# Kernel optimization log

Hardware: AMD Instinct MI355X
Metric: run time of the kernel (lower is better)

## Reference

```python
import jax, jax.numpy as jnp
import numpy as np

N = 100000      # num_nodes
E = 1_600_000   # edges (avg degree 16)
D_IN = 128
D_H = 128
D_OUT = 128


def setup_inputs() -> dict:
    key = jax.random.key(0)
    ks = jax.random.split(key, 11)
    x = jax.random.normal(ks[0], (N, D_IN), dtype=jnp.float32)
    edge_index = jax.random.randint(ks[1], (2, E), 0, N, dtype=jnp.int32)
    s_in = 1.0 / np.sqrt(D_IN)
    s_h = 1.0 / np.sqrt(D_H)
    return {
        "x": x,
        "edge_index": edge_index,
        "W_neigh1": jax.random.uniform(ks[2], (D_H, D_IN), jnp.float32, -s_in, s_in),
        "b_neigh1": jax.random.uniform(ks[3], (D_H,), jnp.float32, -s_in, s_in),
        "W_self1": jax.random.uniform(ks[4], (D_H, D_IN), jnp.float32, -s_in, s_in),
        "b_self1": jax.random.uniform(ks[5], (D_H,), jnp.float32, -s_in, s_in),
        "W_neigh2": jax.random.uniform(ks[6], (D_OUT, D_H), jnp.float32, -s_h, s_h),
        "b_neigh2": jax.random.uniform(ks[7], (D_OUT,), jnp.float32, -s_h, s_h),
        "W_self2": jax.random.uniform(ks[8], (D_OUT, D_H), jnp.float32, -s_h, s_h),
        "b_self2": jax.random.uniform(ks[9], (D_OUT,), jnp.float32, -s_h, s_h),
    }


def reference(x, edge_index, W_neigh1, b_neigh1, W_self1, b_self1,
              W_neigh2, b_neigh2, W_self2, b_self2):
    src, dst = edge_index[0], edge_index[1]
    n = x.shape[0]
    # row-normalized adjacency: deg over dst (row index), clamped to >= 1
    deg = jax.ops.segment_sum(jnp.ones(src.shape[0], x.dtype), dst, num_segments=n)
    inv_deg = 1.0 / jnp.maximum(deg, 1.0)  # [N]

    def agg(h):  # mean aggregation: (A_rownorm @ h)
        return jax.ops.segment_sum(h[src], dst, num_segments=n) * inv_deg[:, None]

    h1 = agg(x) @ W_neigh1.T + b_neigh1 + x @ W_self1.T + b_self1
    h1 = jax.nn.relu(h1)
    # dropout omitted (eval-mode / deterministic reference)
    h2 = agg(h1) @ W_neigh2.T + b_neigh2 + h1 @ W_self2.T + b_self2
    return h2
```

## Files before the change

kernel.cpp:

```cpp
#include <hip/hip_runtime.h>
#include <hip/hip_bf16.h>


typedef __attribute__((ext_vector_type(8))) short short8;
typedef __attribute__((ext_vector_type(4))) float float4_;

#define NBMAX 512

__device__ __forceinline__ unsigned short f2bf(float f) {
    unsigned int u = __float_as_uint(f);
    unsigned int r = (u + 0x7FFFu + ((u >> 16) & 1u)) >> 16;
    return (unsigned short)r;
}

__global__ __launch_bounds__(256) void bucket_count(const int* __restrict__ dst, int E, int NB,
                                                    int* __restrict__ hist) {
    __shared__ int h[NBMAX];
    int tid = threadIdx.x;
    for (int b = tid; b < NB; b += 256) h[b] = 0;
    __syncthreads();
    int base = blockIdx.x * 4096;
    for (int i = 0; i < 16; i++) {
        int e = base + i * 256 + tid;
        if (e < E) atomicAdd(&h[dst[e] >> 8], 1);
    }
    __syncthreads();
    int* out = hist + (size_t)blockIdx.x * NB;
    for (int b = tid; b < NB; b += 256) out[b] = h[b];
}

__global__ __launch_bounds__(256) void blk_scan(const int* __restrict__ hist, int nblk, int NB,
                                                int* __restrict__ baseT,
                                                int* __restrict__ bucketCnt) {
    __shared__ int sd[256];
    __shared__ int carryS;
    int b = blockIdx.x, tid = threadIdx.x;
    if (tid == 0) carryS = 0;
    __syncthreads();
    for (int c0 = 0; c0 < nblk; c0 += 256) {
        int i = c0 + tid;
        int v = (i < nblk) ? hist[(size_t)i * NB + b] : 0;
        sd[tid] = v;
        __syncthreads();
        for (int off = 1; off < 256; off <<= 1) {
            int x = sd[tid];
            int y = (tid >= off) ? sd[tid - off] : 0;
            __syncthreads();
            sd[tid] = x + y;
            __syncthreads();
        }
        int carry = carryS;
        if (i < nblk) baseT[(size_t)i * NB + b] = carry + sd[tid] - v;
        __syncthreads();
        if (tid == 255) carryS = carry + sd[255];
        __syncthreads();
    }
    if (tid == 0) bucketCnt[b] = carryS;
}

__global__ __launch_bounds__(512) void bucket_scan(const int* __restrict__ bucketCnt, int NB,
                                                   int* __restrict__ bucketOffs) {
    __shared__ int sd[512];
    int t = threadIdx.x;
    int v = (t < NB) ? bucketCnt[t] : 0;
    sd[t] = v;
    __syncthreads();
    for (int off = 1; off < 512; off <<= 1) {
        int x = sd[t];
        int y = (t >= off) ? sd[t - off] : 0;
        __syncthreads();
        sd[t] = x + y;
        __syncthreads();
    }
    int excl = sd[t] - v;
    if (t <= NB) bucketOffs[t] = excl;
}

__global__ __launch_bounds__(256) void partition_wprep(
    const int* __restrict__ src, const int* __restrict__ dst, int E, int NB, int partBlocks,
    const int* __restrict__ bucketOffs, const int* __restrict__ baseT,
    unsigned int* __restrict__ bucketBuf,
    const float* __restrict__ Wn1, const float* __restrict__ Ws1,
    const float* __restrict__ bn1, const float* __restrict__ bs1,
    const float* __restrict__ Wn2, const float* __restrict__ Ws2,
    const float* __restrict__ bn2, const float* __restrict__ bs2,
    unsigned short* __restrict__ Bpre, float* __restrict__ biasPre) {
    int tid = threadIdx.x;
    if ((int)blockIdx.x >= partBlocks) {
        int wb = blockIdx.x - partBlocks;
        int l = wb >> 4;
        const float* Wn = l ? Wn2 : Wn1;
        const float* Ws = l ? Ws2 : Ws1;
        int fi = (wb & 15) * 256 + tid;
        int kt = fi >> 9;
        int nt = (fi >> 6) & 7;
        int lane = fi & 63;
        int o = nt * 16 + (lane & 15);
        int k = kt * 32 + (lane >> 4) * 8;
        const float* srcp = (k < 128) ? (Wn + o * 128 + k) : (Ws + o * 128 + (k - 128));
        short8 v;
#pragma unroll
        for (int j = 0; j < 8; j++) v[j] = (short)f2bf(srcp[j]);
        ((short8*)(Bpre + (size_t)l * 32768))[fi] = v;
        if ((wb & 15) == 0 && tid < 128) {
            const float* bn = l ? bn2 : bn1;
            const float* bs = l ? bs2 : bs1;
            biasPre[l * 128 + tid] = bn[tid] + bs[tid];
        }
        return;
    }
    __shared__ int cnt[NBMAX];
    __shared__ int gb[NBMAX];
    for (int b = tid; b < NB; b += 256) {
        cnt[b] = 0;
        gb[b] = bucketOffs[b] + baseT[(size_t)blockIdx.x * NB + b];
    }
    __syncthreads();
    int eb = blockIdx.x * 4096;
    unsigned int pk[16];
    int bk[16], rk[16];
    for (int i = 0; i < 16; i++) {
        int e = eb + i * 256 + tid;
        if (e < E) {
            int d = dst[e];
            bk[i] = d >> 8;
            pk[i] = (unsigned)src[e] | ((unsigned)(d & 255) << 24);
            rk[i] = atomicAdd(&cnt[bk[i]], 1);
        } else {
            bk[i] = -1;
        }
    }
    __syncthreads();
    for (int i = 0; i < 16; i++)
        if (bk[i] >= 0) bucketBuf[gb[bk[i]] + rk[i]] = pk[i];
}

__global__ __launch_bounds__(256) void csrbuild_cvt(
    const unsigned int* __restrict__ bucketBuf, const int* __restrict__ bucketOffs,
    int N, int NB, int* __restrict__ deg, int* __restrict__ offs, int* __restrict__ sortedSrc,
    const float* __restrict__ xin, unsigned int* __restrict__ xb, int n2) {
    int tid = threadIdx.x;
    if ((int)blockIdx.x >= NB) {
        int cb = blockIdx.x - NB;
        int base = cb * 2048 + tid;
        if (xb) {
#pragma unroll
            for (int i = 0; i < 8; i++) {
                int t = base + i * 256;
                if (t < n2) {
                    float2 v = ((const float2*)xin)[t];
                    xb[t] = (unsigned)f2bf(v.x) | ((unsigned)f2bf(v.y) << 16);
                }
            }
        }
        return;
    }
    __shared__ int h[256];
    __shared__ int sc[256];
    __shared__ int cur[256];
    int b = blockIdx.x;
    int n0 = b << 8;
    int bo = bucketOffs[b];
    int cnt = bucketOffs[b + 1] - bo;
    h[tid] = 0;
    __syncthreads();
    for (int i = tid; i < cnt; i += 256) atomicAdd(&h[bucketBuf[bo + i] >> 24], 1);
    __syncthreads();
    int v = h[tid];
    sc[tid] = v;
    __syncthreads();
    for (int off = 1; off < 256; off <<= 1) {
        int x = sc[tid];
        int y = (tid >= off) ? sc[tid - off] : 0;
        __syncthreads();
        sc[tid] = x + y;
        __syncthreads();
    }
    int excl = sc[tid] - v;
    cur[tid] = bo + excl;
    int n = n0 + tid;
    if (n < N) {
        deg[n] = v;
        offs[n] = bo + excl;
    }
    __syncthreads();
    for (int i = tid; i < cnt; i += 256) {
        unsigned int pv = bucketBuf[bo + i];
        int pos = atomicAdd(&cur[pv >> 24], 1);
        sortedSrc[pos] = (int)(pv & 0xFFFFFFu);
    }
}

__global__ __launch_bounds__(256) void agg_bf16_kernel(
    const unsigned int* __restrict__ srcFeats,
    const int* __restrict__ deg, const int* __restrict__ offs,
    const int* __restrict__ sortedSrc,
    unsigned int* __restrict__ dst, int Nn) {
    int wave = threadIdx.x >> 6, lane = threadIdx.x & 63;
    int n = blockIdx.x * 4 + wave;
    if (n >= Nn) return;
    int d = deg[n], st = offs[n];
    float a0 = 0.f, a1 = 0.f;
    int j = 0;
    for (; j + 16 <= d; j += 16) {
        unsigned int uu[16];
#pragma unroll
        for (int u = 0; u < 16; u++) {
            int s = __builtin_amdgcn_readfirstlane(sortedSrc[st + j + u]);
            uu[u] = (srcFeats + (size_t)s * 64)[lane];
        }
#pragma unroll
        for (int u = 0; u < 16; u++) {
            a0 += __uint_as_float(uu[u] << 16);
            a1 += __uint_as_float(uu[u] & 0xFFFF0000u);
        }
    }
    for (; j + 8 <= d; j += 8) {
        unsigned int uu[8];
#pragma unroll
        for (int u = 0; u < 8; u++) {
            int s = __builtin_amdgcn_readfirstlane(sortedSrc[st + j + u]);
            uu[u] = (srcFeats + (size_t)s * 64)[lane];
        }
#pragma unroll
        for (int u = 0; u < 8; u++) {
            a0 += __uint_as_float(uu[u] << 16);
            a1 += __uint_as_float(uu[u] & 0xFFFF0000u);
        }
    }
    for (; j < d; j++) {
        int s = __builtin_amdgcn_readfirstlane(sortedSrc[st + j]);
        unsigned int u = (srcFeats + (size_t)s * 64)[lane];
        a0 += __uint_as_float(u << 16);
        a1 += __uint_as_float(u & 0xFFFF0000u);
    }
    float inv = 1.0f / (float)max(d, 1);
    dst[(size_t)n * 64 + lane] = (unsigned)f2bf(a0 * inv) | ((unsigned)f2bf(a1 * inv) << 16);
}

__global__ __launch_bounds__(256) void agg_f32_kernel(
    const float* __restrict__ srcFeats,
    const int* __restrict__ deg, const int* __restrict__ offs,
    const int* __restrict__ sortedSrc,
    unsigned int* __restrict__ dst, int Nn) {
    int wave = threadIdx.x >> 6, lane = threadIdx.x & 63;
    int n = blockIdx.x * 4 + wave;
    if (n >= Nn) return;
    int d = deg[n], st = offs[n];
    float a0 = 0.f, a1 = 0.f;
    int j = 0;
    for (; j + 8 <= d; j += 8) {
        float2 v[8];
#pragma unroll
        for (int u = 0; u < 8; u++) {
            int s = __builtin_amdgcn_readfirstlane(sortedSrc[st + j + u]);
            v[u] = ((const float2*)(srcFeats + (size_t)s * 128))[lane];
        }
#pragma unroll
        for (int u = 0; u < 8; u++) {
            a0 += v[u].x;
            a1 += v[u].y;
        }
    }
    for (; j < d; j++) {
        int s = __builtin_amdgcn_readfirstlane(sortedSrc[st + j]);
        float2 v = ((const float2*)(srcFeats + (size_t)s * 128))[lane];
        a0 += v.x;
        a1 += v.y;
    }
    float inv = 1.0f / (float)max(d, 1);
    dst[(size_t)n * 64 + lane] = (unsigned)f2bf(a0 * inv) | ((unsigned)f2bf(a1 * inv) << 16);
}

__global__ __launch_bounds__(256) void gemm_kernel(
    const unsigned short* __restrict__ Aagg, const void* Aself,
    const unsigned short* __restrict__ Bpre, const float* __restrict__ biasPre,
    void* Out, int relu, int selfF32, int outBf16, int Nrows) {
    __shared__ unsigned short ldsB[8 * 8 * 64 * 8];
    __shared__ float biasS[128];
    int tid = threadIdx.x;

#pragma unroll
    for (int i = 0; i < 16; i++) {
        int fi = tid + 256 * i;
        ((short8*)ldsB)[fi] = ((const short8*)Bpre)[fi];
    }
    if (tid < 128) biasS[tid] = biasPre[tid];
    __syncthreads();

    int wave = tid >> 6, lane = tid & 63;
    int quad = lane >> 4, mr = lane & 15;
    int rowBase = blockIdx.x * 128 + wave * 32;

    float4_ acc[2][8];
    float4_ z = {0.f, 0.f, 0.f, 0.f};
    for (int mt = 0; mt < 2; mt++)
        for (int nt = 0; nt < 8; nt++) acc[mt][nt] = z;

    for (int kt = 0; kt < 8; kt++) {
        int kk = (kt & 3) * 32 + quad * 8;
        short8 a[2];
        for (int mt = 0; mt < 2; mt++) {
            int row = rowBase + mt * 16 + mr;
            if (row >= Nrows) row = Nrows - 1;
            if (kt < 4) {
                a[mt] = *(const short8*)(Aagg + (size_t)row * 128 + kk);
            } else if (selfF32) {
                const float* p = (const float*)Aself + (size_t)row * 128 + kk;
                float4_ f0 = *(const float4_*)p;
                float4_ f1 = *(const float4_*)(p + 4);
                short8 t;
#pragma unroll
                for (int j = 0; j < 4; j++) {
                    t[j] = (short)f2bf(f0[j]);
                    t[4 + j] = (short)f2bf(f1[j]);
                }
                a[mt] = t;
            } else {
                a[mt] = *(const short8*)((const unsigned short*)Aself + (size_t)row * 128 + kk);
            }
        }
        for (int nt = 0; nt < 8; nt++) {
            short8 b = *(const short8*)(ldsB + ((size_t)(kt * 8 + nt) * 64 + lane) * 8);
            acc[0][nt] = __builtin_amdgcn_mfma_f32_16x16x32_bf16(a[0], b, acc[0][nt], 0, 0, 0);
            acc[1][nt] = __builtin_amdgcn_mfma_f32_16x16x32_bf16(a[1], b, acc[1][nt], 0, 0, 0);
        }
    }

    for (int mt = 0; mt < 2; mt++) {
        for (int nt = 0; nt < 8; nt++) {
            int col = nt * 16 + mr;
            float bv = biasS[col];
            for (int r = 0; r < 4; r++) {
                int row = rowBase + mt * 16 + quad * 4 + r;
                if (row < Nrows) {
                    float v = acc[mt][nt][r] + bv;
                    if (relu) v = fmaxf(v, 0.f);
                    if (outBf16)
                        ((unsigned short*)Out)[(size_t)row * 128 + col] = f2bf(v);
                    else
                        ((float*)Out)[(size_t)row * 128 + col] = v;
                }
            }
        }
    }
}

extern "C" void kernel_launch(void* const* d_in, const int* in_sizes, int n_in,
                              void* d_out, int out_size, void* d_ws, size_t ws_size,
                              hipStream_t stream) {
    const float* x = (const float*)d_in[0];
    const int* ei = (const int*)d_in[1];
    const float* Wn1 = (const float*)d_in[2];
    const float* bn1 = (const float*)d_in[3];
    const float* Ws1 = (const float*)d_in[4];
    const float* bs1 = (const float*)d_in[5];
    const float* Wn2 = (const float*)d_in[6];
    const float* bn2 = (const float*)d_in[7];
    const float* Ws2 = (const float*)d_in[8];
    const float* bs2 = (const float*)d_in[9];

    const int N = in_sizes[0] / 128;
    const int E = in_sizes[1] / 2;
    const int* srcI = ei;
    const int* dstI = ei + E;
    const int NB = (N + 255) >> 8;
    const int ebBlocks = (E + 4095) / 4096;

    char* ws = (char*)d_ws;
    size_t off = 0;
    auto alloc = [&](size_t bytes) -> void* {
        void* p = ws + off;
        off += (bytes + 255) & ~(size_t)255;
        return p;
    };
    int* deg = (int*)alloc((size_t)N * 4);
    int* offs = (int*)alloc((size_t)N * 4);
    int* bucketCnt = (int*)alloc((NBMAX + 1) * 4);
    int* bucketOffs = (int*)alloc((NBMAX + 1) * 4);
    int* hist = (int*)alloc((size_t)ebBlocks * NB * 4);
    int* baseT = (int*)alloc((size_t)ebBlocks * NB * 4);
    unsigned short* Bpre = (unsigned short*)alloc(2 * 32768 * 2);
    float* biasPre = (float*)alloc(2 * 128 * 4);
    int* sortedSrc = (int*)alloc((size_t)E * 4);
    unsigned short* Aagg = (unsigned short*)alloc((size_t)N * 128 * 2);
    size_t baseNeed = off;
    size_t bf16Buf = ((size_t)N * 128 * 2 + 255) & ~(size_t)255;
    bool bigWs = (ws_size >= baseNeed + 2 * bf16Buf);
    unsigned int* xb = nullptr;
    unsigned short* h1b = nullptr;
    if (bigWs) {
        xb = (unsigned int*)alloc((size_t)N * 128 * 2);
        h1b = (unsigned short*)alloc((size_t)N * 128 * 2);
    }
    unsigned int* bucketBuf = (unsigned int*)Aagg;

    int n2 = N * 64;
    int cvtBlocks = bigWs ? (n2 + 2047) / 2048 : 0;
    bucket_count<<<ebBlocks, 256, 0, stream>>>(dstI, E, NB, hist);
    blk_scan<<<NB, 256, 0, stream>>>(hist, ebBlocks, NB, baseT, bucketCnt);
    bucket_scan<<<1, 512, 0, stream>>>(bucketCnt, NB, bucketOffs);
    partition_wprep<<<ebBlocks + 32, 256, 0, stream>>>(
        srcI, dstI, E, NB, ebBlocks, bucketOffs, baseT, bucketBuf,
        Wn1, Ws1, bn1, bs1, Wn2, Ws2, bn2, bs2, Bpre, biasPre);
    csrbuild_cvt<<<NB + cvtBlocks, 256, 0, stream>>>(bucketBuf, bucketOffs, N, NB, deg, offs,
                                                     sortedSrc, x, xb, n2);

    int aggBlocks = (N + 3) / 4;
    int gemmBlocks = (N + 127) / 128;

    if (bigWs) {
        agg_bf16_kernel<<<aggBlocks, 256, 0, stream>>>(xb, deg, offs, sortedSrc,
                                                       (unsigned int*)Aagg, N);
        gemm_kernel<<<gemmBlocks, 256, 0, stream>>>(Aagg, xb, Bpre, biasPre, h1b, 1, 0, 1, N);
        agg_bf16_kernel<<<aggBlocks, 256, 0, stream>>>((const unsigned int*)h1b, deg, offs,
                                                       sortedSrc, (unsigned int*)Aagg, N);
        gemm_kernel<<<gemmBlocks, 256, 0, stream>>>(Aagg, h1b, Bpre + 32768, biasPre + 128,
                                                    d_out, 0, 0, 0, N);
    } else {
        float* h1 = (float*)d_out;
        agg_f32_kernel<<<aggBlocks, 256, 0, stream>>>(x, deg, offs, sortedSrc,
                                                      (unsigned int*)Aagg, N);
        gemm_kernel<<<gemmBlocks, 256, 0, stream>>>(Aagg, x, Bpre, biasPre, h1, 1, 1, 0, N);
        agg_f32_kernel<<<aggBlocks, 256, 0, stream>>>(h1, deg, offs, sortedSrc,
                                                      (unsigned int*)Aagg, N);
        gemm_kernel<<<gemmBlocks, 256, 0, stream>>>(Aagg, h1, Bpre + 32768, biasPre + 128,
                                                    d_out, 0, 1, 0, N);
    }
}
```

Before: 347.1 us.

## Fuse CSR build kernels into one persistent kernel with grid barriers

Merges the five preprocessing launches (bucket count, block scan, bucket scan, partition with weight prep, CSR build with x conversion) into a single persistent kernel of G blocks that uses atomic-counter grid barriers between phases. This removes per-launch overhead and the idle tails between small kernels. The grid barrier assumes every block is co-resident, which is not guaranteed by the launch. Phases that ran wide before now loop over chunks with fewer blocks, which may reduce parallelism.

```diff
diff --git a/kernel.cpp b/kernel.cpp
--- a/kernel.cpp
+++ b/kernel.cpp
@@ -13,81 +13,51 @@
     return (unsigned short)r;
 }
 
-__global__ __launch_bounds__(256) void bucket_count(const int* __restrict__ dst, int E, int NB,
-                                                    int* __restrict__ hist) {
-    __shared__ int h[NBMAX];
-    int tid = threadIdx.x;
-    for (int b = tid; b < NB; b += 256) h[b] = 0;
+__device__ __forceinline__ void gbar(int* bar, int id, int G) {
     __syncthreads();
-    int base = blockIdx.x * 4096;
-    for (int i = 0; i < 16; i++) {
-        int e = base + i * 256 + tid;
-        if (e < E) atomicAdd(&h[dst[e] >> 8], 1);
+    if (threadIdx.x == 0) {
+        __threadfence();
+        atomicAdd(&bar[id], 1);
+        while (atomicAdd(&bar[id], 0) < G) __builtin_amdgcn_s_sleep(16);
+        __threadfence();
     }
     __syncthreads();
-    int* out = hist + (size_t)blockIdx.x * NB;
-    for (int b = tid; b < NB; b += 256) out[b] = h[b];
-}
-
-__global__ __launch_bounds__(256) void blk_scan(const int* __restrict__ hist, int nblk, int NB,
-                                                int* __restrict__ baseT,
-                                                int* __restrict__ bucketCnt) {
-    __shared__ int sd[256];
-    __shared__ int carryS;
-    int b = blockIdx.x, tid = threadIdx.x;
-    if (tid == 0) carryS = 0;
-    __syncthreads();
-    for (int c0 = 0; c0 < nblk; c0 += 256) {
-        int i = c0 + tid;
-        int v = (i < nblk) ? hist[(size_t)i * NB + b] : 0;
-        sd[tid] = v;
-        __syncthreads();
-        for (int off = 1; off < 256; off <<= 1) {
-            int x = sd[tid];
-            int y = (tid >= off) ? sd[tid - off] : 0;
-            __syncthreads();
-            sd[tid] = x + y;
-            __syncthreads();
-        }
-        int carry = carryS;
-        if (i < nblk) baseT[(size_t)i * NB + b] = carry + sd[tid] - v;
-        __syncthreads();
-        if (tid == 255) carryS = carry + sd[255];
-        __syncthreads();
-    }
-    if (tid == 0) bucketCnt[b] = carryS;
-}
-
-__global__ __launch_bounds__(512) void bucket_scan(const int* __restrict__ bucketCnt, int NB,
-                                                   int* __restrict__ bucketOffs) {
-    __shared__ int sd[512];
-    int t = threadIdx.x;
-    int v = (t < NB) ? bucketCnt[t] : 0;
-    sd[t] = v;
-    __syncthreads();
-    for (int off = 1; off < 512; off <<= 1) {
-        int x = sd[t];
-        int y = (t >= off) ? sd[t - off] : 0;
-        __syncthreads();
-        sd[t] = x + y;
-        __syncthreads();
-    }
-    int excl = sd[t] - v;
-    if (t <= NB) bucketOffs[t] = excl;
-}
-
-__global__ __launch_bounds__(256) void partition_wprep(
-    const int* __restrict__ src, const int* __restrict__ dst, int E, int NB, int partBlocks,
-    const int* __restrict__ bucketOffs, const int* __restrict__ baseT,
+}
+
+__global__ __launch_bounds__(256, 4) void mega_csr(
+    const int* __restrict__ src, const int* __restrict__ dst, int E, int N, int NB, int CHK,
+    int G, int* __restrict__ bar, int* __restrict__ hist, int* __restrict__ baseT,
+    int* __restrict__ bucketCnt, int* __restrict__ bucketOffs,
     unsigned int* __restrict__ bucketBuf,
+    int* __restrict__ deg, int* __restrict__ offs, int* __restrict__ sortedSrc,
+    const float* __restrict__ xin, unsigned int* __restrict__ xb, int n2,
     const float* __restrict__ Wn1, const float* __restrict__ Ws1,
     const float* __restrict__ bn1, const float* __restrict__ bs1,
     const float* __restrict__ Wn2, const float* __restrict__ Ws2,
     const float* __restrict__ bn2, const float* __restrict__ bs2,
     unsigned short* __restrict__ Bpre, float* __restrict__ biasPre) {
+    __shared__ int h[NBMAX];
+    __shared__ int sc[256];
+    __shared__ int cur[256];
+    __shared__ int gb[NBMAX];
     int tid = threadIdx.x;
-    if ((int)blockIdx.x >= partBlocks) {
-        int wb = blockIdx.x - partBlocks;
+    int bb = blockIdx.x;
+
+    for (int c = bb; c < CHK; c += G) {
+        for (int b = tid; b < NB; b += 256) h[b] = 0;
+        __syncthreads();
+        int base = c * 4096;
+        for (int i = 0; i < 16; i++) {
+            int e = base + i * 256 + tid;
+            if (e < E) atomicAdd(&h[dst[e] >> 8], 1);
+        }
+        __syncthreads();
+        int* out = hist + (size_t)c * NB;
+        for (int b = tid; b < NB; b += 256) out[b] = h[b];
+        __syncthreads();
+    }
+    if (bb < 32) {
+        int wb = bb;
         int l = wb >> 4;
         const float* Wn = l ? Wn2 : Wn1;
         const float* Ws = l ? Ws2 : Ws1;
@@ -107,87 +77,130 @@
             const float* bs = l ? bs2 : bs1;
             biasPre[l * 128 + tid] = bn[tid] + bs[tid];
         }
-        return;
-    }
-    __shared__ int cnt[NBMAX];
-    __shared__ int gb[NBMAX];
-    for (int b = tid; b < NB; b += 256) {
-        cnt[b] = 0;
-        gb[b] = bucketOffs[b] + baseT[(size_t)blockIdx.x * NB + b];
-    }
-    __syncthreads();
-    int eb = blockIdx.x * 4096;
-    unsigned int pk[16];
-    int bk[16], rk[16];
-    for (int i = 0; i < 16; i++) {
-        int e = eb + i * 256 + tid;
-        if (e < E) {
-            int d = dst[e];
-            bk[i] = d >> 8;
-            pk[i] = (unsigned)src[e] | ((unsigned)(d & 255) << 24);
-            rk[i] = atomicAdd(&cnt[bk[i]], 1);
-        } else {
-            bk[i] = -1;
-        }
-    }
-    __syncthreads();
-    for (int i = 0; i < 16; i++)
-        if (bk[i] >= 0) bucketBuf[gb[bk[i]] + rk[i]] = pk[i];
-}
-
-__global__ __launch_bounds__(256) void csrbuild_cvt(
-    const unsigned int* __restrict__ bucketBuf, const int* __restrict__ bucketOffs,
-    int N, int NB, int* __restrict__ deg, int* __restrict__ offs, int* __restrict__ sortedSrc,
-    const float* __restrict__ xin, unsigned int* __restrict__ xb, int n2) {
-    int tid = threadIdx.x;
-    if ((int)blockIdx.x >= NB) {
-        int cb = blockIdx.x - NB;
-        int base = cb * 2048 + tid;
-        if (xb) {
-#pragma unroll
-            for (int i = 0; i < 8; i++) {
-                int t = base + i * 256;
-                if (t < n2) {
-                    float2 v = ((const float2*)xin)[t];
-                    xb[t] = (unsigned)f2bf(v.x) | ((unsigned)f2bf(v.y) << 16);
-                }
+    }
+    if (xb) {
+        for (int t = bb * 256 + tid; t < n2; t += G * 256) {
+            float2 v = ((const float2*)xin)[t];
+            xb[t] = (unsigned)f2bf(v.x) | ((unsigned)f2bf(v.y) << 16);
+        }
+    }
+    gbar(bar, 0, G);
+
+    if (bb < NB) {
+        int carry = 0;
+        for (int c0 = 0; c0 < CHK; c0 += 256) {
+            int i = c0 + tid;
+            int v = (i < CHK) ? hist[(size_t)i * NB + bb] : 0;
+            sc[tid] = v;
+            __syncthreads();
+            for (int off = 1; off < 256; off <<= 1) {
+                int x = sc[tid];
+                int y = (tid >= off) ? sc[tid - off] : 0;
+                __syncthreads();
+                sc[tid] = x + y;
+                __syncthreads();
             }
-        }
-        return;
-    }
-    __shared__ int h[256];
-    __shared__ int sc[256];
-    __shared__ int cur[256];
-    int b = blockIdx.x;
-    int n0 = b << 8;
-    int bo = bucketOffs[b];
-    int cnt = bucketOffs[b + 1] - bo;
-    h[tid] = 0;
-    __syncthreads();
-    for (int i = tid; i < cnt; i += 256) atomicAdd(&h[bucketBuf[bo + i] >> 24], 1);
-    __syncthreads();
-    int v = h[tid];
-    sc[tid] = v;
-    __syncthreads();
-    for (int off = 1; off < 256; off <<= 1) {
-        int x = sc[tid];
-        int y = (tid >= off) ? sc[tid - off] : 0;
-        __syncthreads();
-        sc[tid] = x + y;
-        __syncthreads();
-    }
-    int excl = sc[tid] - v;
-    cur[tid] = bo + excl;
-    int n = n0 + tid;
-    if (n < N) {
-        deg[n] = v;
-        offs[n] = bo + excl;
-    }
-    __syncthreads();
-    for (int i = tid; i < cnt; i += 256) {
-        unsigned int pv = bucketBuf[bo + i];
-        int pos = atomicAdd(&cur[pv >> 24], 1);
-        sortedSrc[pos] = (int)(pv & 0xFFFFFFu);
+            if (i < CHK) baseT[(size_t)i * NB + bb] = carry + sc[tid] - v;
+            carry += sc[255];
+            __syncthreads();
+        }
+        if (tid == 0) bucketCnt[bb] = carry;
+    }
+    gbar(bar, 1, G);
+
+    if (bb == 0) {
+        int v0 = (tid < NB) ? bucketCnt[tid] : 0;
+        int j = 256 + tid;
+        int v1 = (j < NB) ? bucketCnt[j] : 0;
+        sc[tid] = v0;
+        __syncthreads();
+        for (int off = 1; off < 256; off <<= 1) {
+            int x = sc[tid];
+            int y = (tid >= off) ? sc[tid - off] : 0;
+            __syncthreads();
+            sc[tid] = x + y;
+            __syncthreads();
+        }
+        int inc0 = sc[tid];
+        int tot0 = sc[255];
+        __syncthreads();
+        sc[tid] = v1;
+        __syncthreads();
+        for (int off = 1; off < 256; off <<= 1) {
+            int x = sc[tid];
+            int y = (tid >= off) ? sc[tid - off] : 0;
+            __syncthreads();
+            sc[tid] = x + y;
+            __syncthreads();
+        }
+        int inc1 = sc[tid];
+        int tot1 = sc[255];
+        __syncthreads();
+        if (tid < NB) bucketOffs[tid] = inc0 - v0;
+        if (j < NB) bucketOffs[j] = tot0 + inc1 - v1;
+        if (tid == 0) bucketOffs[NB] = tot0 + tot1;
+    }
+    gbar(bar, 2, G);
+
+    for (int c = bb; c < CHK; c += G) {
+        for (int b = tid; b < NB; b += 256) {
+            h[b] = 0;
+            gb[b] = bucketOffs[b] + baseT[(size_t)c * NB + b];
+        }
+        __syncthreads();
+        int eb = c * 4096;
+        unsigned int pk[16];
+        int bk[16], rk[16];
+        for (int i = 0; i < 16; i++) {
+            int e = eb + i * 256 + tid;
+            if (e < E) {
+                int d = dst[e];
+                bk[i] = d >> 8;
+                pk[i] = (unsigned)src[e] | ((unsigned)(d & 255) << 24);
+                rk[i] = atomicAdd(&h[bk[i]], 1);
+            } else {
+                bk[i] = -1;
+            }
+        }
+        __syncthreads();
+        for (int i = 0; i < 16; i++)
+            if (bk[i] >= 0) bucketBuf[gb[bk[i]] + rk[i]] = pk[i];
+        __syncthreads();
+    }
+    gbar(bar, 3, G);
+
+    if (bb < NB) {
+        int b = bb;
+        int n0 = b << 8;
+        int bo = bucketOffs[b];
+        int cnt = bucketOffs[b + 1] - bo;
+        h[tid] = 0;
+        __syncthreads();
+        for (int i = tid; i < cnt; i += 256) atomicAdd(&h[bucketBuf[bo + i] >> 24], 1);
+        __syncthreads();
+        int v = h[tid];
+        sc[tid] = v;
+        __syncthreads();
+        for (int off = 1; off < 256; off <<= 1) {
+            int x = sc[tid];
+            int y = (tid >= off) ? sc[tid - off] : 0;
+            __syncthreads();
+            sc[tid] = x + y;
+            __syncthreads();
+        }
+        int excl = sc[tid] - v;
+        cur[tid] = bo + excl;
+        int n = n0 + tid;
+        if (n < N) {
+            deg[n] = v;
+            offs[n] = bo + excl;
+        }
+        __syncthreads();
+        for (int i = tid; i < cnt; i += 256) {
+            unsigned int pv = bucketBuf[bo + i];
+            int pos = atomicAdd(&cur[pv >> 24], 1);
+            sortedSrc[pos] = (int)(pv & 0xFFFFFFu);
+        }
     }
 }
 
@@ -365,7 +378,11 @@
     const int* srcI = ei;
     const int* dstI = ei + E;
     const int NB = (N + 255) >> 8;
-    const int ebBlocks = (E + 4095) / 4096;
+    const int CHK = (E + 4095) / 4096;
+
+    int G = NB > 32 ? NB : 32;
+    if (CHK > G) G = CHK;
+    if (G > 1024) G = 1024;
 
     char* ws = (char*)d_ws;
     size_t off = 0;
@@ -378,8 +395,9 @@
     int* offs = (int*)alloc((size_t)N * 4);
     int* bucketCnt = (int*)alloc((NBMAX + 1) * 4);
     int* bucketOffs = (int*)alloc((NBMAX + 1) * 4);
-    int* hist = (int*)alloc((size_t)ebBlocks * NB * 4);
-    int* baseT = (int*)alloc((size_t)ebBlocks * NB * 4);
+    int* bar = (int*)alloc(16 * 4);
+    int* hist = (int*)alloc((size_t)CHK * NB * 4);
+    int* baseT = (int*)alloc((size_t)CHK * NB * 4);
     unsigned short* Bpre = (unsigned short*)alloc(2 * 32768 * 2);
     float* biasPre = (float*)alloc(2 * 128 * 4);
     int* sortedSrc = (int*)alloc((size_t)E * 4);
@@ -396,15 +414,11 @@
     unsigned int* bucketBuf = (unsigned int*)Aagg;
 
     int n2 = N * 64;
-    int cvtBlocks = bigWs ? (n2 + 2047) / 2048 : 0;
-    bucket_count<<<ebBlocks, 256, 0, stream>>>(dstI, E, NB, hist);
-    blk_scan<<<NB, 256, 0, stream>>>(hist, ebBlocks, NB, baseT, bucketCnt);
-    bucket_scan<<<1, 512, 0, stream>>>(bucketCnt, NB, bucketOffs);
-    partition_wprep<<<ebBlocks + 32, 256, 0, stream>>>(
-        srcI, dstI, E, NB, ebBlocks, bucketOffs, baseT, bucketBuf,
-        Wn1, Ws1, bn1, bs1, Wn2, Ws2, bn2, bs2, Bpre, biasPre);
-    csrbuild_cvt<<<NB + cvtBlocks, 256, 0, stream>>>(bucketBuf, bucketOffs, N, NB, deg, offs,
-                                                     sortedSrc, x, xb, n2);
+    hipMemsetAsync(bar, 0, 64, stream);
+    mega_csr<<<G, 256, 0, stream>>>(srcI, dstI, E, N, NB, CHK, G, bar, hist, baseT,
+                                    bucketCnt, bucketOffs, bucketBuf, deg, offs, sortedSrc,
+                                    x, xb, n2, Wn1, Ws1, bn1, bs1, Wn2, Ws2, bn2, bs2,
+                                    Bpre, biasPre);
 
     int aggBlocks = (N + 3) / 4;
     int gemmBlocks = (N + 127) / 128;
```

Result: slower. 519.5 us (+49.7%).

## Fuse aggregation and GEMM into persistent kernels with grid barrier; inline bucket scan

Applied to the files above, without the earlier changes.

Replaces each separate aggregation and GEMM launch pair with one persistent kernel of 512 blocks. Each block first gathers mean-aggregated neighbour features, then meets the others at a global atomic barrier, then runs the MFMA GEMM tiles. The single-block bucket_scan launch is removed: every partition and CSR-build block now recomputes the bucket prefix sum itself in shared memory. This cuts launch count and inter-kernel gaps. In exchange it adds redundant scan work, a spin barrier that needs all 512 blocks resident at once (deadlock risk otherwise), and persistent-grid load imbalance.

```diff
diff --git a/kernel.cpp b/kernel.cpp
--- a/kernel.cpp
+++ b/kernel.cpp
@@ -11,6 +11,17 @@
     unsigned int u = __float_as_uint(f);
     unsigned int r = (u + 0x7FFFu + ((u >> 16) & 1u)) >> 16;
     return (unsigned short)r;
+}
+
+__device__ __forceinline__ void gbar(int* bar, int id, int G) {
+    __syncthreads();
+    if (threadIdx.x == 0) {
+        __threadfence();
+        atomicAdd(&bar[id], 1);
+        while (atomicAdd(&bar[id], 0) < G) __builtin_amdgcn_s_sleep(16);
+        __threadfence();
+    }
+    __syncthreads();
 }
 
 __global__ __launch_bounds__(256) void bucket_count(const int* __restrict__ dst, int E, int NB,
@@ -31,10 +42,12 @@
 
 __global__ __launch_bounds__(256) void blk_scan(const int* __restrict__ hist, int nblk, int NB,
                                                 int* __restrict__ baseT,
-                                                int* __restrict__ bucketCnt) {
+                                                int* __restrict__ bucketCnt,
+                                                int* __restrict__ bar) {
     __shared__ int sd[256];
     __shared__ int carryS;
     int b = blockIdx.x, tid = threadIdx.x;
+    if (b == 0 && tid < 16) bar[tid] = 0;
     if (tid == 0) carryS = 0;
     __syncthreads();
     for (int c0 = 0; c0 < nblk; c0 += 256) {
@@ -58,27 +71,31 @@
     if (tid == 0) bucketCnt[b] = carryS;
 }
 
-__global__ __launch_bounds__(512) void bucket_scan(const int* __restrict__ bucketCnt, int NB,
-                                                   int* __restrict__ bucketOffs) {
-    __shared__ int sd[512];
-    int t = threadIdx.x;
-    int v = (t < NB) ? bucketCnt[t] : 0;
-    sd[t] = v;
-    __syncthreads();
-    for (int off = 1; off < 512; off <<= 1) {
-        int x = sd[t];
-        int y = (t >= off) ? sd[t - off] : 0;
-        __syncthreads();
-        sd[t] = x + y;
-        __syncthreads();
-    }
-    int excl = sd[t] - v;
-    if (t <= NB) bucketOffs[t] = excl;
+__device__ __forceinline__ void scan_buckets(const int* __restrict__ bucketCnt, int NB,
+                                             int* bOffs, int* sc) {
+    int tid = threadIdx.x;
+    int b0 = 2 * tid, b1 = 2 * tid + 1;
+    int c0 = (b0 < NB) ? bucketCnt[b0] : 0;
+    int c1 = (b1 < NB) ? bucketCnt[b1] : 0;
+    int ts = c0 + c1;
+    sc[tid] = ts;
+    __syncthreads();
+    for (int off = 1; off < 256; off <<= 1) {
+        int x = sc[tid];
+        int y = (tid >= off) ? sc[tid - off] : 0;
+        __syncthreads();
+        sc[tid] = x + y;
+        __syncthreads();
+    }
+    int excl = sc[tid] - ts;
+    bOffs[b0] = excl;
+    bOffs[b1] = excl + c0;
+    __syncthreads();
 }
 
 __global__ __launch_bounds__(256) void partition_wprep(
     const int* __restrict__ src, const int* __restrict__ dst, int E, int NB, int partBlocks,
-    const int* __restrict__ bucketOffs, const int* __restrict__ baseT,
+    const int* __restrict__ bucketCnt, const int* __restrict__ baseT,
     unsigned int* __restrict__ bucketBuf,
     const float* __restrict__ Wn1, const float* __restrict__ Ws1,
     const float* __restrict__ bn1, const float* __restrict__ bs1,
@@ -110,10 +127,13 @@
         return;
     }
     __shared__ int cnt[NBMAX];
+    __shared__ int bOffs[NBMAX];
     __shared__ int gb[NBMAX];
+    __shared__ int sc[256];
+    scan_buckets(bucketCnt, NB, bOffs, sc);
     for (int b = tid; b < NB; b += 256) {
         cnt[b] = 0;
-        gb[b] = bucketOffs[b] + baseT[(size_t)blockIdx.x * NB + b];
+        gb[b] = bOffs[b] + baseT[(size_t)blockIdx.x * NB + b];
     }
     __syncthreads();
     int eb = blockIdx.x * 4096;
@@ -136,7 +156,7 @@
 }
 
 __global__ __launch_bounds__(256) void csrbuild_cvt(
-    const unsigned int* __restrict__ bucketBuf, const int* __restrict__ bucketOffs,
+    const unsigned int* __restrict__ bucketBuf, const int* __restrict__ bucketCnt,
     int N, int NB, int* __restrict__ deg, int* __restrict__ offs, int* __restrict__ sortedSrc,
     const float* __restrict__ xin, unsigned int* __restrict__ xb, int n2) {
     int tid = threadIdx.x;
@@ -155,13 +175,15 @@
         }
         return;
     }
+    __shared__ int bOffs[NBMAX];
     __shared__ int h[256];
     __shared__ int sc[256];
     __shared__ int cur[256];
+    scan_buckets(bucketCnt, NB, bOffs, sc);
     int b = blockIdx.x;
     int n0 = b << 8;
-    int bo = bucketOffs[b];
-    int cnt = bucketOffs[b + 1] - bo;
+    int bo = bOffs[b];
+    int cnt = bucketCnt[b];
     h[tid] = 0;
     __syncthreads();
     for (int i = tid; i < cnt; i += 256) atomicAdd(&h[bucketBuf[bo + i] >> 24], 1);
@@ -191,51 +213,110 @@
     }
 }
 
-__global__ __launch_bounds__(256) void agg_bf16_kernel(
-    const unsigned int* __restrict__ srcFeats,
+__global__ __launch_bounds__(256) void fused_agg_gemm(
+    const unsigned int* __restrict__ table,
     const int* __restrict__ deg, const int* __restrict__ offs,
-    const int* __restrict__ sortedSrc,
-    unsigned int* __restrict__ dst, int Nn) {
-    int wave = threadIdx.x >> 6, lane = threadIdx.x & 63;
-    int n = blockIdx.x * 4 + wave;
-    if (n >= Nn) return;
-    int d = deg[n], st = offs[n];
-    float a0 = 0.f, a1 = 0.f;
-    int j = 0;
-    for (; j + 16 <= d; j += 16) {
-        unsigned int uu[16];
-#pragma unroll
-        for (int u = 0; u < 16; u++) {
-            int s = __builtin_amdgcn_readfirstlane(sortedSrc[st + j + u]);
-            uu[u] = (srcFeats + (size_t)s * 64)[lane];
-        }
-#pragma unroll
-        for (int u = 0; u < 16; u++) {
-            a0 += __uint_as_float(uu[u] << 16);
-            a1 += __uint_as_float(uu[u] & 0xFFFF0000u);
-        }
-    }
-    for (; j + 8 <= d; j += 8) {
-        unsigned int uu[8];
-#pragma unroll
-        for (int u = 0; u < 8; u++) {
-            int s = __builtin_amdgcn_readfirstlane(sortedSrc[st + j + u]);
-            uu[u] = (srcFeats + (size_t)s * 64)[lane];
-        }
-#pragma unroll
-        for (int u = 0; u < 8; u++) {
-            a0 += __uint_as_float(uu[u] << 16);
-            a1 += __uint_as_float(uu[u] & 0xFFFF0000u);
-        }
-    }
-    for (; j < d; j++) {
-        int s = __builtin_amdgcn_readfirstlane(sortedSrc[st + j]);
-        unsigned int u = (srcFeats + (size_t)s * 64)[lane];
-        a0 += __uint_as_float(u << 16);
-        a1 += __uint_as_float(u & 0xFFFF0000u);
-    }
-    float inv = 1.0f / (float)max(d, 1);
-    dst[(size_t)n * 64 + lane] = (unsigned)f2bf(a0 * inv) | ((unsigned)f2bf(a1 * inv) << 16);
+    const int* __restrict__ sortedSrc, unsigned int* __restrict__ Aagg,
+    const unsigned short* __restrict__ Bpre, const float* __restrict__ biasPre,
+    void* Out, int relu, int outBf16, int Nn, int G, int* __restrict__ bar, int barId) {
+    __shared__ unsigned short ldsB[32768];
+    __shared__ float biasS[128];
+    int tid = threadIdx.x;
+
+#pragma unroll
+    for (int i = 0; i < 16; i++) {
+        int fi = tid + 256 * i;
+        ((short8*)ldsB)[fi] = ((const short8*)Bpre)[fi];
+    }
+    if (tid < 128) biasS[tid] = biasPre[tid];
+
+    int wave = tid >> 6, lane = tid & 63;
+
+    for (int n = blockIdx.x * 4 + wave; n < Nn; n += G * 4) {
+        int d = deg[n], st = offs[n];
+        float a0 = 0.f, a1 = 0.f;
+        int j = 0;
+        for (; j + 16 <= d; j += 16) {
+            unsigned int uu[16];
+#pragma unroll
+            for (int u = 0; u < 16; u++) {
+                int s = __builtin_amdgcn_readfirstlane(sortedSrc[st + j + u]);
+                uu[u] = (table + (size_t)s * 64)[lane];
+            }
+#pragma unroll
+            for (int u = 0; u < 16; u++) {
+                a0 += __uint_as_float(uu[u] << 16);
+                a1 += __uint_as_float(uu[u] & 0xFFFF0000u);
+            }
+        }
+        for (; j + 8 <= d; j += 8) {
+            unsigned int uu[8];
+#pragma unroll
+            for (int u = 0; u < 8; u++) {
+                int s = __builtin_amdgcn_readfirstlane(sortedSrc[st + j + u]);
+                uu[u] = (table + (size_t)s * 64)[lane];
+            }
+#pragma unroll
+            for (int u = 0; u < 8; u++) {
+                a0 += __uint_as_float(uu[u] << 16);
+                a1 += __uint_as_float(uu[u] & 0xFFFF0000u);
+            }
+        }
+        for (; j < d; j++) {
+            int s = __builtin_amdgcn_readfirstlane(sortedSrc[st + j]);
+            unsigned int u = (table + (size_t)s * 64)[lane];
+            a0 += __uint_as_float(u << 16);
+            a1 += __uint_as_float(u & 0xFFFF0000u);
+        }
+        float inv = 1.0f / (float)max(d, 1);
+        Aagg[(size_t)n * 64 + lane] = (unsigned)f2bf(a0 * inv) | ((unsigned)f2bf(a1 * inv) << 16);
+    }
+
+    gbar(bar, barId, G);
+
+    int quad = lane >> 4, mr = lane & 15;
+    const unsigned short* Aa = (const unsigned short*)Aagg;
+    const unsigned short* As = (const unsigned short*)table;
+    int nTiles = (Nn + 127) >> 7;
+    for (int t = blockIdx.x; t < nTiles; t += G) {
+        int rowBase = t * 128 + wave * 32;
+        float4_ acc[2][8];
+        float4_ z = {0.f, 0.f, 0.f, 0.f};
+        for (int mt = 0; mt < 2; mt++)
+            for (int nt = 0; nt < 8; nt++) acc[mt][nt] = z;
+        for (int kt = 0; kt < 8; kt++) {
+            int kk = (kt & 3) * 32 + quad * 8;
+            short8 a[2];
+            for (int mt = 0; mt < 2; mt++) {
+                int row = rowBase + mt * 16 + mr;
+                if (row >= Nn) row = Nn - 1;
+                const unsigned short* ap = (kt < 4) ? Aa : As;
+                a[mt] = *(const short8*)(ap + (size_t)row * 128 + kk);
+            }
+            for (int nt = 0; nt < 8; nt++) {
+                short8 b = *(const short8*)(ldsB + ((size_t)(kt * 8 + nt) * 64 + lane) * 8);
+                acc[0][nt] = __builtin_amdgcn_mfma_f32_16x16x32_bf16(a[0], b, acc[0][nt], 0, 0, 0);
+                acc[1][nt] = __builtin_amdgcn_mfma_f32_16x16x32_bf16(a[1], b, acc[1][nt], 0, 0, 0);
+            }
+        }
+        for (int mt = 0; mt < 2; mt++) {
+            for (int nt = 0; nt < 8; nt++) {
+                int col = nt * 16 + mr;
+                float bv = biasS[col];
+                for (int r = 0; r < 4; r++) {
+                    int row = rowBase + mt * 16 + quad * 4 + r;
+                    if (row < Nn) {
+                        float v = acc[mt][nt][r] + bv;
+                        if (relu) v = fmaxf(v, 0.f);
+                        if (outBf16)
+                            ((unsigned short*)Out)[(size_t)row * 128 + col] = f2bf(v);
+                        else
+                            ((float*)Out)[(size_t)row * 128 + col] = v;
+                    }
+                }
+            }
+        }
+    }
 }
 
 __global__ __launch_bounds__(256) void agg_f32_kernel(
@@ -279,7 +360,6 @@
     __shared__ unsigned short ldsB[8 * 8 * 64 * 8];
     __shared__ float biasS[128];
     int tid = threadIdx.x;
-
 #pragma unroll
     for (int i = 0; i < 16; i++) {
         int fi = tid + 256 * i;
@@ -326,7 +406,6 @@
             acc[1][nt] = __builtin_amdgcn_mfma_f32_16x16x32_bf16(a[1], b, acc[1][nt], 0, 0, 0);
         }
     }
-
     for (int mt = 0; mt < 2; mt++) {
         for (int nt = 0; nt < 8; nt++) {
             int col = nt * 16 + mr;
@@ -377,7 +456,7 @@
     int* deg = (int*)alloc((size_t)N * 4);
     int* offs = (int*)alloc((size_t)N * 4);
     int* bucketCnt = (int*)alloc((NBMAX + 1) * 4);
-    int* bucketOffs = (int*)alloc((NBMAX + 1) * 4);
+    int* bar = (int*)alloc(16 * 4);
     int* hist = (int*)alloc((size_t)ebBlocks * NB * 4);
     int* baseT = (int*)alloc((size_t)ebBlocks * NB * 4);
     unsigned short* Bpre = (unsigned short*)alloc(2 * 32768 * 2);
@@ -398,26 +477,24 @@
     int n2 = N * 64;
     int cvtBlocks = bigWs ? (n2 + 2047) / 2048 : 0;
     bucket_count<<<ebBlocks, 256, 0, stream>>>(dstI, E, NB, hist);
-    blk_scan<<<NB, 256, 0, stream>>>(hist, ebBlocks, NB, baseT, bucketCnt);
-    bucket_scan<<<1, 512, 0, stream>>>(bucketCnt, NB, bucketOffs);
+    blk_scan<<<NB, 256, 0, stream>>>(hist, ebBlocks, NB, baseT, bucketCnt, bar);
     partition_wprep<<<ebBlocks + 32, 256, 0, stream>>>(
-        srcI, dstI, E, NB, ebBlocks, bucketOffs, baseT, bucketBuf,
+        srcI, dstI, E, NB, ebBlocks, bucketCnt, baseT, bucketBuf,
         Wn1, Ws1, bn1, bs1, Wn2, Ws2, bn2, bs2, Bpre, biasPre);
-    csrbuild_cvt<<<NB + cvtBlocks, 256, 0, stream>>>(bucketBuf, bucketOffs, N, NB, deg, offs,
+    csrbuild_cvt<<<NB + cvtBlocks, 256, 0, stream>>>(bucketBuf, bucketCnt, N, NB, deg, offs,
                                                      sortedSrc, x, xb, n2);
 
-    int aggBlocks = (N + 3) / 4;
-    int gemmBlocks = (N + 127) / 128;
-
     if (bigWs) {
-        agg_bf16_kernel<<<aggBlocks, 256, 0, stream>>>(xb, deg, offs, sortedSrc,
-                                                       (unsigned int*)Aagg, N);
-        gemm_kernel<<<gemmBlocks, 256, 0, stream>>>(Aagg, xb, Bpre, biasPre, h1b, 1, 0, 1, N);
-        agg_bf16_kernel<<<aggBlocks, 256, 0, stream>>>((const unsigned int*)h1b, deg, offs,
-                                                       sortedSrc, (unsigned int*)Aagg, N);
-        gemm_kernel<<<gemmBlocks, 256, 0, stream>>>(Aagg, h1b, Bpre + 32768, biasPre + 128,
-                                                    d_out, 0, 0, 0, N);
+        const int G = 512;
+        fused_agg_gemm<<<G, 256, 0, stream>>>(xb, deg, offs, sortedSrc,
+                                              (unsigned int*)Aagg, Bpre, biasPre,
+                                              h1b, 1, 1, N, G, bar, 0);
+        fused_agg_gemm<<<G, 256, 0, stream>>>((const unsigned int*)h1b, deg, offs, sortedSrc,
+                                              (unsigned int*)Aagg, Bpre + 32768, biasPre + 128,
+                                              d_out, 0, 0, N, G, bar, 1);
     } else {
+        int aggBlocks = (N + 3) / 4;
+        int gemmBlocks = (N + 127) / 128;
         float* h1 = (float*)d_out;
         agg_f32_kernel<<<aggBlocks, 256, 0, stream>>>(x, deg, offs, sortedSrc,
                                                       (unsigned int*)Aagg, N);
```

After: 613.5 us. 76.8% more time.

## Fold bucket scan into partition/CSR kernels and preload GEMM A fragments

Applied to the files above, without the earlier changes.

Drops the single-block bucket_scan launch. Each partition and CSR-build block now recomputes the bucket prefix sum redundantly in shared memory from bucketCnt. This removes one kernel launch and its serialization point, at the cost of extra per-block scan work. Separately, the GEMM kernel now loads all A fragments for the eight k-steps up front and fully unrolls the MFMA loop, so loads can issue early, at the cost of more registers.

```diff
diff --git a/kernel.cpp b/kernel.cpp
--- a/kernel.cpp
+++ b/kernel.cpp
@@ -58,27 +58,31 @@
     if (tid == 0) bucketCnt[b] = carryS;
 }
 
-__global__ __launch_bounds__(512) void bucket_scan(const int* __restrict__ bucketCnt, int NB,
-                                                   int* __restrict__ bucketOffs) {
-    __shared__ int sd[512];
-    int t = threadIdx.x;
-    int v = (t < NB) ? bucketCnt[t] : 0;
-    sd[t] = v;
-    __syncthreads();
-    for (int off = 1; off < 512; off <<= 1) {
-        int x = sd[t];
-        int y = (t >= off) ? sd[t - off] : 0;
-        __syncthreads();
-        sd[t] = x + y;
-        __syncthreads();
-    }
-    int excl = sd[t] - v;
-    if (t <= NB) bucketOffs[t] = excl;
+__device__ __forceinline__ void scan_buckets(const int* __restrict__ bucketCnt, int NB,
+                                             int* bOffs, int* sc) {
+    int tid = threadIdx.x;
+    int b0 = 2 * tid, b1 = 2 * tid + 1;
+    int c0 = (b0 < NB) ? bucketCnt[b0] : 0;
+    int c1 = (b1 < NB) ? bucketCnt[b1] : 0;
+    int ts = c0 + c1;
+    sc[tid] = ts;
+    __syncthreads();
+    for (int off = 1; off < 256; off <<= 1) {
+        int x = sc[tid];
+        int y = (tid >= off) ? sc[tid - off] : 0;
+        __syncthreads();
+        sc[tid] = x + y;
+        __syncthreads();
+    }
+    int excl = sc[tid] - ts;
+    bOffs[b0] = excl;
+    bOffs[b1] = excl + c0;
+    __syncthreads();
 }
 
 __global__ __launch_bounds__(256) void partition_wprep(
     const int* __restrict__ src, const int* __restrict__ dst, int E, int NB, int partBlocks,
-    const int* __restrict__ bucketOffs, const int* __restrict__ baseT,
+    const int* __restrict__ bucketCnt, const int* __restrict__ baseT,
     unsigned int* __restrict__ bucketBuf,
     const float* __restrict__ Wn1, const float* __restrict__ Ws1,
     const float* __restrict__ bn1, const float* __restrict__ bs1,
@@ -110,10 +114,13 @@
         return;
     }
     __shared__ int cnt[NBMAX];
+    __shared__ int bOffs[NBMAX];
     __shared__ int gb[NBMAX];
+    __shared__ int sc[256];
+    scan_buckets(bucketCnt, NB, bOffs, sc);
     for (int b = tid; b < NB; b += 256) {
         cnt[b] = 0;
-        gb[b] = bucketOffs[b] + baseT[(size_t)blockIdx.x * NB + b];
+        gb[b] = bOffs[b] + baseT[(size_t)blockIdx.x * NB + b];
     }
     __syncthreads();
     int eb = blockIdx.x * 4096;
@@ -136,7 +143,7 @@
 }
 
 __global__ __launch_bounds__(256) void csrbuild_cvt(
-    const unsigned int* __restrict__ bucketBuf, const int* __restrict__ bucketOffs,
+    const unsigned int* __restrict__ bucketBuf, const int* __restrict__ bucketCnt,
     int N, int NB, int* __restrict__ deg, int* __restrict__ offs, int* __restrict__ sortedSrc,
     const float* __restrict__ xin, unsigned int* __restrict__ xb, int n2) {
     int tid = threadIdx.x;
@@ -155,13 +162,15 @@
         }
         return;
     }
+    __shared__ int bOffs[NBMAX];
     __shared__ int h[256];
     __shared__ int sc[256];
     __shared__ int cur[256];
+    scan_buckets(bucketCnt, NB, bOffs, sc);
     int b = blockIdx.x;
     int n0 = b << 8;
-    int bo = bucketOffs[b];
-    int cnt = bucketOffs[b + 1] - bo;
+    int bo = bOffs[b];
+    int cnt = bucketCnt[b];
     h[tid] = 0;
     __syncthreads();
     for (int i = tid; i < cnt; i += 256) atomicAdd(&h[bucketBuf[bo + i] >> 24], 1);
@@ -292,38 +301,49 @@
     int quad = lane >> 4, mr = lane & 15;
     int rowBase = blockIdx.x * 128 + wave * 32;
 
-    float4_ acc[2][8];
-    float4_ z = {0.f, 0.f, 0.f, 0.f};
-    for (int mt = 0; mt < 2; mt++)
-        for (int nt = 0; nt < 8; nt++) acc[mt][nt] = z;
-
-    for (int kt = 0; kt < 8; kt++) {
-        int kk = (kt & 3) * 32 + quad * 8;
-        short8 a[2];
-        for (int mt = 0; mt < 2; mt++) {
-            int row = rowBase + mt * 16 + mr;
-            if (row >= Nrows) row = Nrows - 1;
-            if (kt < 4) {
-                a[mt] = *(const short8*)(Aagg + (size_t)row * 128 + kk);
-            } else if (selfF32) {
-                const float* p = (const float*)Aself + (size_t)row * 128 + kk;
-                float4_ f0 = *(const float4_*)p;
-                float4_ f1 = *(const float4_*)(p + 4);
+    short8 af[2][8];
+#pragma unroll
+    for (int mt = 0; mt < 2; mt++) {
+        int row = rowBase + mt * 16 + mr;
+        if (row >= Nrows) row = Nrows - 1;
+        const unsigned short* pa = Aagg + (size_t)row * 128 + quad * 8;
+#pragma unroll
+        for (int kt = 0; kt < 4; kt++) af[mt][kt] = *(const short8*)(pa + kt * 32);
+        if (selfF32) {
+            const float* ps = (const float*)Aself + (size_t)row * 128 + quad * 8;
+#pragma unroll
+            for (int kt = 0; kt < 4; kt++) {
+                float4_ f0 = *(const float4_*)(ps + kt * 32);
+                float4_ f1 = *(const float4_*)(ps + kt * 32 + 4);
                 short8 t;
 #pragma unroll
                 for (int j = 0; j < 4; j++) {
                     t[j] = (short)f2bf(f0[j]);
                     t[4 + j] = (short)f2bf(f1[j]);
                 }
-                a[mt] = t;
-            } else {
-                a[mt] = *(const short8*)((const unsigned short*)Aself + (size_t)row * 128 + kk);
+                af[mt][4 + kt] = t;
             }
-        }
+        } else {
+            const unsigned short* ps = (const unsigned short*)Aself + (size_t)row * 128 + quad * 8;
+#pragma unroll
+            for (int kt = 0; kt < 4; kt++) af[mt][4 + kt] = *(const short8*)(ps + kt * 32);
+        }
+    }
+
+    float4_ acc[2][8];
+    float4_ z = {0.f, 0.f, 0.f, 0.f};
+#pragma unroll
+    for (int mt = 0; mt < 2; mt++)
+#pragma unroll
+        for (int nt = 0; nt < 8; nt++) acc[mt][nt] = z;
+
+#pragma unroll
+    for (int kt = 0; kt < 8; kt++) {
+#pragma unroll
         for (int nt = 0; nt < 8; nt++) {
             short8 b = *(const short8*)(ldsB + ((size_t)(kt * 8 + nt) * 64 + lane) * 8);
-            acc[0][nt] = __builtin_amdgcn_mfma_f32_16x16x32_bf16(a[0], b, acc[0][nt], 0, 0, 0);
-            acc[1][nt] = __builtin_amdgcn_mfma_f32_16x16x32_bf16(a[1], b, acc[1][nt], 0, 0, 0);
+            acc[0][nt] = __builtin_amdgcn_mfma_f32_16x16x32_bf16(af[0][kt], b, acc[0][nt], 0, 0, 0);
+            acc[1][nt] = __builtin_amdgcn_mfma_f32_16x16x32_bf16(af[1][kt], b, acc[1][nt], 0, 0, 0);
         }
     }
 
@@ -377,7 +397,6 @@
     int* deg = (int*)alloc((size_t)N * 4);
     int* offs = (int*)alloc((size_t)N * 4);
     int* bucketCnt = (int*)alloc((NBMAX + 1) * 4);
-    int* bucketOffs = (int*)alloc((NBMAX + 1) * 4);
     int* hist = (int*)alloc((size_t)ebBlocks * NB * 4);
     int* baseT = (int*)alloc((size_t)ebBlocks * NB * 4);
     unsigned short* Bpre = (unsigned short*)alloc(2 * 32768 * 2);
@@ -399,11 +418,10 @@
     int cvtBlocks = bigWs ? (n2 + 2047) / 2048 : 0;
     bucket_count<<<ebBlocks, 256, 0, stream>>>(dstI, E, NB, hist);
     blk_scan<<<NB, 256, 0, stream>>>(hist, ebBlocks, NB, baseT, bucketCnt);
-    bucket_scan<<<1, 512, 0, stream>>>(bucketCnt, NB, bucketOffs);
     partition_wprep<<<ebBlocks + 32, 256, 0, stream>>>(
-        srcI, dstI, E, NB, ebBlocks, bucketOffs, baseT, bucketBuf,
+        srcI, dstI, E, NB, ebBlocks, bucketCnt, baseT, bucketBuf,
         Wn1, Ws1, bn1, bs1, Wn2, Ws2, bn2, bs2, Bpre, biasPre);
-    csrbuild_cvt<<<NB + cvtBlocks, 256, 0, stream>>>(bucketBuf, bucketOffs, N, NB, deg, offs,
+    csrbuild_cvt<<<NB + cvtBlocks, 256, 0, stream>>>(bucketBuf, bucketCnt, N, NB, deg, offs,
                                                      sortedSrc, x, xb, n2);
 
     int aggBlocks = (N + 3) / 4;
```

Result: no change. 348.2 us (+0.3%).
